# Performance work log

Measured on AMD Instinct MI355X. Metric: run time of the kernel, lower is better.

## Reference

```python
import jax, jax.numpy as jnp
import numpy as np

NMS_PRE_MAXSIZE = 4096
NMS_POST_MAXSIZE = 512
NMS_THRESH = 0.7


def setup_inputs() -> dict:
    key = jax.random.key(0)
    k1, k2, k3, k4, k5 = jax.random.split(key, 5)
    B, N, C = 4, 32768, 3
    # realistic 3D boxes: (x, y, z, dx, dy, dz, heading)
    xy = jax.random.uniform(k1, (B, N, 2), dtype=jnp.float32) * 70.0
    z = jax.random.uniform(k2, (B, N, 1), dtype=jnp.float32) * 4.0 - 2.0
    sizes = jax.random.uniform(k3, (B, N, 3), dtype=jnp.float32) * 3.0 + 1.0
    heading = jax.random.uniform(k4, (B, N, 1), dtype=jnp.float32) * 6.2832 - 3.1416
    batch_box_preds = jnp.concatenate([xy, z, sizes, heading], axis=-1)  # (B,N,7)
    batch_cls_preds = jax.random.uniform(k5, (B, N, C), dtype=jnp.float32)  # (B,N,3)
    return {"batch_box_preds": batch_box_preds, "batch_cls_preds": batch_cls_preds}


def _nms_single(boxes, scores, labels):
    # boxes (N,7), scores (N,), labels (N,) int32
    top_s, idx = jax.lax.top_k(scores, NMS_PRE_MAXSIZE)   # sort desc, keep pre-maxsize
    b = boxes[idx]                                        # (PRE,7)
    l = labels[idx]
    # BEV axis-aligned IoU (reference surrogate for the rotated-BEV CUDA IoU kernel)
    x, y, dx, dy = b[:, 0], b[:, 1], b[:, 3], b[:, 4]
    x1, x2 = x - 0.5 * dx, x + 0.5 * dx
    y1, y2 = y - 0.5 * dy, y + 0.5 * dy
    area = dx * dy
    ix = jnp.maximum(0.0, jnp.minimum(x2[:, None], x2[None, :]) - jnp.maximum(x1[:, None], x1[None, :]))
    iy = jnp.maximum(0.0, jnp.minimum(y2[:, None], y2[None, :]) - jnp.maximum(y1[:, None], y1[None, :]))
    inter = ix * iy
    iou = jax.lax.stop_gradient(inter / (area[:, None] + area[None, :] - inter + 1e-6))

    ar = jnp.arange(NMS_PRE_MAXSIZE)

    def body(i, keep):
        sup = (iou[i] > NMS_THRESH) & (ar > i) & keep[i]
        return keep & ~sup

    keep = jax.lax.fori_loop(0, NMS_PRE_MAXSIZE, body, jnp.ones(NMS_PRE_MAXSIZE, bool))

    # pack first NMS_POST_MAXSIZE kept boxes into fixed-size zero-padded outputs
    rank = jnp.cumsum(keep) - 1
    valid = keep & (rank < NMS_POST_MAXSIZE)
    pos = jnp.where(valid, rank, NMS_POST_MAXSIZE)  # invalid -> scratch row
    rois = jnp.zeros((NMS_POST_MAXSIZE + 1, 7), b.dtype).at[pos].set(b)[:NMS_POST_MAXSIZE]
    sc = jnp.zeros((NMS_POST_MAXSIZE + 1,), top_s.dtype).at[pos].set(top_s)[:NMS_POST_MAXSIZE]
    lb = jnp.zeros((NMS_POST_MAXSIZE + 1,), jnp.int32).at[pos].set(l)[:NMS_POST_MAXSIZE]
    return rois, sc, lb


def reference(batch_box_preds, batch_cls_preds):
    # per-box max score / argmax class (torch.max(cls_preds, dim=1) per sample)
    roi_scores_all = jnp.max(batch_cls_preds, axis=-1)                 # (B,N)
    roi_labels_all = jnp.argmax(batch_cls_preds, axis=-1).astype(jnp.int32)
    rois, roi_scores, roi_labels = jax.vmap(_nms_single)(batch_box_preds, roi_scores_all, roi_labels_all)
    return rois, roi_scores, roi_labels + 1  # labels shifted by +1 as in proposal_layer
```

## Files before the change

kernel.cpp:

```cpp
#include <hip/hip_runtime.h>
#include <stdint.h>

#define BB 4
#define NN 32768
#define PRE 4096
#define POST 512
#define NMS_TH 0.7f
#define MIDCAP 8192
#define P1G 16

typedef unsigned long long u64;
typedef unsigned int u32;

__device__ __forceinline__ u32 orderable(float f) {
  u32 u = __float_as_uint(f);
  return (u & 0x80000000u) ? ~u : (u | 0x80000000u);
}
__device__ __forceinline__ float unorderable(u32 o) {
  u32 u = (o & 0x80000000u) ? (o & 0x7fffffffu) : ~o;
  return __uint_as_float(u);
}
__device__ __forceinline__ u32 bucket_of(float s) {
  u32 v = (u32)(s * 2147483648.0f);
  u32 bk = v >> 20;
  return bk > 2047u ? 2047u : bk;
}
__device__ __forceinline__ u64 readlane64(u64 v, int l) {
  u32 lo = (u32)__builtin_amdgcn_readlane((int)(u32)v, l);
  u32 hi = (u32)__builtin_amdgcn_readlane((int)(u32)(v >> 32), l);
  return ((u64)hi << 32) | lo;
}

__global__ void zero_kernel(u32* __restrict__ hist, u32* __restrict__ cnt_mid) {
  int t = blockIdx.x * 256 + threadIdx.x;
  if (t < BB * 2048) hist[t] = 0;
  if (t < BB) cnt_mid[t] = 0;
}

__global__ __launch_bounds__(256) void score_hist_kernel(const float* __restrict__ cls,
                                                         int* __restrict__ labels,
                                                         u64* __restrict__ keys,
                                                         u32* __restrict__ hist) {
  __shared__ u32 lh[2048];
  for (int t = threadIdx.x; t < 2048; t += 256) lh[t] = 0;
  __syncthreads();
  int g = blockIdx.x * 256 + threadIdx.x;
  const float* c = cls + (size_t)g * 3;
  float s = c[0]; int l = 0;
  float c1 = c[1], c2 = c[2];
  if (c1 > s) { s = c1; l = 1; }
  if (c2 > s) { s = c2; l = 2; }
  int n = g & (NN - 1);
  keys[g] = ((u64)orderable(s) << 32) | (u32)(~(u32)n);
  labels[g] = l;
  atomicAdd(&lh[bucket_of(s)], 1u);
  __syncthreads();
  int b = blockIdx.x >> 7;
  for (int t = threadIdx.x; t < 2048; t += 256) {
    u32 v = lh[t];
    if (v) atomicAdd(&hist[b * 2048 + t], v);
  }
}

__global__ __launch_bounds__(256) void select_kernel(const u32* __restrict__ hist,
                                                     u32* __restrict__ selinfo,
                                                     u32* __restrict__ sfxBuf,
                                                     u32* __restrict__ cursor) {
  __shared__ u32 sfx[2048];
  int b = blockIdx.x;
  for (int t = threadIdx.x; t < 2048; t += 256) sfx[t] = hist[b * 2048 + t];
  __syncthreads();
  for (int d = 1; d < 2048; d <<= 1) {
    u32 v[8];
#pragma unroll
    for (int i = 0; i < 8; ++i) {
      int t = threadIdx.x + i * 256;
      v[i] = (t + d < 2048) ? sfx[t + d] : 0;
    }
    __syncthreads();
#pragma unroll
    for (int i = 0; i < 8; ++i) sfx[threadIdx.x + i * 256] += v[i];
    __syncthreads();
  }
  for (int t = threadIdx.x; t < 2048; t += 256) {
    u32 above = (t + 1 < 2048) ? sfx[t + 1] : 0;
    sfxBuf[b * 2048 + t] = sfx[t];
    cursor[b * 2048 + t] = above;
    if (above < PRE && sfx[t] >= PRE) { selinfo[b * 2] = (u32)t; selinfo[b * 2 + 1] = above; }
  }
}

__global__ __launch_bounds__(256) void compact_kernel(const u64* __restrict__ keys,
                                                      const u32* __restrict__ selinfo,
                                                      u32* __restrict__ cursor,
                                                      u64* __restrict__ sel, u64* __restrict__ mid,
                                                      u32* __restrict__ cnt_mid) {
  int g = blockIdx.x * 256 + threadIdx.x;
  int b = g >> 15;
  u64 key = keys[g];
  u32 bk = bucket_of(unorderable((u32)(key >> 32)));
  u32 T = selinfo[b * 2];
  if (bk > T) {
    u32 p = atomicAdd(&cursor[b * 2048 + bk], 1u);
    sel[((size_t)b << 12) + p] = key;
  } else if (bk == T) {
    u32 p = atomicAdd(&cnt_mid[b], 1u);
    if (p < MIDCAP) mid[(size_t)b * MIDCAP + p] = key;
  }
}

__global__ __launch_bounds__(64) void bsort_kernel(u64* __restrict__ sel, u64* __restrict__ mid,
                                                   const u32* __restrict__ sfxBuf,
                                                   const u32* __restrict__ selinfo,
                                                   const u32* __restrict__ cnt_mid,
                                                   const float* __restrict__ boxes,
                                                   const int* __restrict__ labels,
                                                   float* __restrict__ topBox,
                                                   float4* __restrict__ P,
                                                   float* __restrict__ AR,
                                                   float* __restrict__ topS,
                                                   int* __restrict__ topL) {
  int t = blockIdx.x & 2047;
  int b = blockIdx.x >> 11;
  int lane = threadIdx.x;
  u32 T = selinfo[b * 2];
  if ((u32)t < T) return;
  u64* selB = sel + ((size_t)b << 12);
  u32 start, end;
  if ((u32)t == T) {
    u32 C1 = selinfo[b * 2 + 1];
    int need = PRE - (int)C1;
    int M = (int)cnt_mid[b]; if (M > MIDCAP) M = MIDCAP;
    u64* midB = mid + (size_t)b * MIDCAP;
    for (int r = 0; r < need; ++r) {
      u64 best = 0; int bi = -1;
      for (int q = lane; q < M; q += 64) {
        u64 v = midB[q];
        if (v > best) { best = v; bi = q; }
      }
#pragma unroll
      for (int d = 32; d > 0; d >>= 1) {
        u64 ob = __shfl_xor(best, d, 64);
        int oi = __shfl_xor(bi, d, 64);
        if (ob > best) { best = ob; bi = oi; }
      }
      if (lane == 0) selB[C1 + r] = best;
      if (bi >= 0 && lane == (bi & 63)) midB[bi] = 0;
    }
    start = C1; end = PRE;
  } else {
    start = (t < 2047) ? sfxBuf[b * 2048 + t + 1] : 0u;
    end = sfxBuf[b * 2048 + t];
    int n = (int)(end - start);
    if (n > 64) {
      for (int r = 0; r < n - 1; ++r) {
        u64 best = 0; int bi = -1;
        for (int q = r + lane; q < n; q += 64) {
          u64 v = selB[start + q];
          if (v > best) { best = v; bi = q; }
        }
#pragma unroll
        for (int d = 32; d > 0; d >>= 1) {
          u64 ob = __shfl_xor(best, d, 64);
          int oi = __shfl_xor(bi, d, 64);
          if (ob > best) { best = ob; bi = oi; }
        }
        if (lane == 0) {
          u64 tmp = selB[start + r];
          selB[start + r] = best;
          selB[start + bi] = tmp;
        }
      }
    } else if (n > 1) {
      u64 v = (lane < n) ? selB[start + lane] : 0ULL;
#pragma unroll
      for (int k = 2; k <= 64; k <<= 1) {
#pragma unroll
        for (int j = k >> 1; j > 0; j >>= 1) {
          u64 o = __shfl_xor(v, j, 64);
          bool up = ((lane & k) == 0);
          bool first = ((lane & j) == 0);
          u64 mx = v > o ? v : o, mn = v > o ? o : v;
          v = (first == up) ? mx : mn;
        }
      }
      if (lane < n) selB[start + lane] = v;
    }
  }
  __builtin_amdgcn_s_waitcnt(0);
  for (u32 pos = start + lane; pos < end; pos += 64) {
    u64 key = selB[pos];
    u32 n = ~(u32)key;
    size_t src = (size_t)b * NN + n;
    const float* bx = boxes + src * 7;
    float x = bx[0], y = bx[1], dx = bx[3], dy = bx[4];
    size_t gidx = ((size_t)b << 12) + pos;
    float* tb = topBox + gidx * 7;
#pragma unroll
    for (int c = 0; c < 7; ++c) tb[c] = bx[c];
    float4 p;
    p.x = x - 0.5f * dx; p.z = x + 0.5f * dx;
    p.y = y - 0.5f * dy; p.w = y + 0.5f * dy;
    P[gidx] = p;
    AR[gidx] = dx * dy;
    topS[gidx] = unorderable((u32)(key >> 32));
    topL[gidx] = labels[src];
  }
}

__device__ __forceinline__ void mask_tile(int b, int rb, int w, int lane,
                                          const float4* __restrict__ P,
                                          const float* __restrict__ AR,
                                          u64* __restrict__ maskT,
                                          u64* __restrict__ diag) {
  int base = b << 12;
  int row = (rb << 6) + lane;
  float4 rp = P[base + row];
  float rar = AR[base + row];
  const float4* __restrict__ Pcol = P + base + (w << 6);
  const float* __restrict__ ARcol = AR + base + (w << 6);
  u64 bits = 0;
  float margMin = 1.0f;
#pragma unroll 8
  for (int k = 0; k < 64; ++k) {
    float4 cb = Pcol[k];
    float ca = ARcol[k];
    float ix = fminf(rp.z, cb.z) - fmaxf(rp.x, cb.x); ix = fmaxf(0.0f, ix);
    float iy = fminf(rp.w, cb.w) - fmaxf(rp.y, cb.y); iy = fmaxf(0.0f, iy);
    float inter = ix * iy;
    float denom = ((rar + ca) - inter) + 1e-6f;
    float t = 0.7f * denom;
    bits |= ((u64)(inter > t ? 1u : 0u)) << k;
    margMin = fminf(margMin, fabsf(inter - t) - 2e-5f * t);
  }
  if (__any(margMin <= 0.0f)) {
    bits = 0;
    for (int k = 0; k < 64; ++k) {
      float4 cb = Pcol[k];
      float ca = ARcol[k];
      float ix = fminf(rp.z, cb.z) - fmaxf(rp.x, cb.x); ix = fmaxf(0.0f, ix);
      float iy = fminf(rp.w, cb.w) - fmaxf(rp.y, cb.y); iy = fmaxf(0.0f, iy);
      float inter = ix * iy;
      float denom = ((rar + ca) - inter) + 1e-6f;
      bits |= ((u64)(((inter / denom) > NMS_TH) ? 1u : 0u)) << k;
    }
  }
  maskT[((size_t)(b * 64 + w)) * PRE + row] = bits;
  if (w == rb) diag[base + row] = bits;
}

__global__ __launch_bounds__(256) void mask1_kernel(const float4* __restrict__ P,
                                                    const float* __restrict__ AR,
                                                    u64* __restrict__ maskT,
                                                    u64* __restrict__ diag) {
  int b = blockIdx.y;
  int ti = blockIdx.x * 4 + (threadIdx.x >> 6);
  int lane = threadIdx.x & 63;
  int rb = 0;
  while (rb < P1G - 1 && (64 * (rb + 1) - ((rb + 1) * rb) / 2) <= ti) ++rb;
  int w = rb + (ti - (64 * rb - (rb * (rb - 1)) / 2));
  mask_tile(b, rb, w, lane, P, AR, maskT, diag);
}

__global__ __launch_bounds__(256) void mask2_kernel(const float4* __restrict__ P,
                                                    const float* __restrict__ AR,
                                                    u64* __restrict__ maskT,
                                                    u64* __restrict__ diag,
                                                    const u32* __restrict__ doneFlag) {
  int b = blockIdx.y;
  if (doneFlag[b]) return;
  int ti = blockIdx.x * 4 + (threadIdx.x >> 6);
  int lane = threadIdx.x & 63;
  int rr = 0;
  while (rr < 47 && (48 * (rr + 1) - ((rr + 1) * rr) / 2) <= ti) ++rr;
  int rb = rr + P1G;
  int w = rb + (ti - (48 * rr - (rr * (rr - 1)) / 2));
  mask_tile(b, rb, w, lane, P, AR, maskT, diag);
}

__global__ __launch_bounds__(64, 1) void scan_kernel(const u64* __restrict__ maskT,
                                                     const u64* __restrict__ diag,
                                                     const float* __restrict__ topBox,
                                                     const float* __restrict__ topS,
                                                     const int* __restrict__ topL,
                                                     float* __restrict__ out,
                                                     u64* __restrict__ rState,
                                                     u64* __restrict__ kwState,
                                                     u32* __restrict__ nkState,
                                                     u32* __restrict__ doneFlag,
                                                     int phase) {
  __shared__ u64 kwLDS[64];
  int b = blockIdx.x;
  int lane = threadIdx.x;
  if (phase == 1 && doneFlag[b]) return;
  const u64* m = maskT + (size_t)b * 64 * PRE;
  const u64* dg = diag + (size_t)b * PRE;
  u64 r; int nk, gs, ge;
  if (phase == 0) {
    kwLDS[lane] = 0; r = 0; nk = 0; gs = 0; ge = P1G;
  } else {
    kwLDS[lane] = (lane < P1G) ? kwState[b * 64 + lane] : 0;
    r = rState[b * 64 + lane]; nk = nkState[b]; gs = P1G; ge = 64;
  }
  __syncthreads();
  bool done = false;
  u64 d_next = dg[(size_t)gs * 64 + lane];
  for (int g = gs; g < ge; ++g) {
    u64 d_cur = d_next;
    if (g + 1 < ge) d_next = dg[(size_t)(g + 1) * 64 + lane];
    u64 sup = readlane64(r, g);
    u64 keep;
    u64 anyd = __ballot(d_cur != 0ULL);
    if (anyd == 0ULL) {
      keep = ~sup;
    } else {
      keep = 0;
#pragma unroll
      for (int k = 0; k < 64; ++k) {
        u64 dk = readlane64(d_cur, k);
        u64 bit = (sup >> k) & 1ULL;
        keep |= (bit ^ 1ULL) << k;
        sup |= (dk & ~((2ULL << k) - 1ULL)) & (bit - 1ULL);
      }
    }
    const ulonglong2* mp = (const ulonglong2*)(m + (size_t)lane * PRE + ((size_t)g << 6));
    u64 acc = 0;
#pragma unroll
    for (int q = 0; q < 32; ++q) {
      ulonglong2 v = mp[q];
      u64 g0 = 0ULL - ((keep >> (2 * q)) & 1ULL);
      u64 g1 = 0ULL - ((keep >> (2 * q + 1)) & 1ULL);
      acc |= (v.x & g0) | (v.y & g1);
    }
    r |= acc;
    if (lane == 0) kwLDS[g] = keep;
    nk += (int)__popcll(keep);
    if (nk >= POST) { done = true; break; }
  }
  __syncthreads();
  if (phase == 0 && !done) {
    rState[b * 64 + lane] = r;
    if (lane < P1G) kwState[b * 64 + lane] = kwLDS[lane];
    if (lane == 0) { nkState[b] = nk; doneFlag[b] = 0; }
    return;
  }
  if (phase == 0 && lane == 0) doneFlag[b] = 1;
  u64 kw = kwLDS[lane];
  int cnt = __popcll(kw);
  int pfx = cnt;
#pragma unroll
  for (int d = 1; d < 64; d <<= 1) {
    int up = __shfl_up(pfx, d, 64);
    if (lane >= d) pfx += up;
  }
  int total = __shfl(pfx, 63, 64);
  int pos = pfx - cnt;
  float* outR = out;
  float* outS = out + BB * POST * 7;
  float* outL = outS + BB * POST;
  while (kw) {
    int t = __ffsll((long long)kw) - 1;
    kw &= kw - 1;
    if (pos < POST) {
      int i = (lane << 6) + t;
      int g = (b << 9) + pos;
      const float* tb = topBox + ((size_t)(b << 12) + i) * 7;
#pragma unroll
      for (int c = 0; c < 7; ++c) outR[(size_t)g * 7 + c] = tb[c];
      outS[g] = topS[(b << 12) + i];
      outL[g] = (float)(topL[(b << 12) + i] + 1);
    }
    ++pos;
  }
  int fin = total < POST ? total : POST;
  for (int s = fin + lane; s < POST; s += 64) {
    int g = (b << 9) + s;
#pragma unroll
    for (int c = 0; c < 7; ++c) outR[(size_t)g * 7 + c] = 0.0f;
    outS[g] = 0.0f;
    outL[g] = 1.0f;
  }
}

extern "C" void kernel_launch(void* const* d_in, const int* in_sizes, int n_in,
                              void* d_out, int out_size, void* d_ws, size_t ws_size,
                              hipStream_t stream) {
  const float* boxes = (const float*)d_in[0];
  const float* cls   = (const float*)d_in[1];
  float* out = (float*)d_out;

  char* p = (char*)d_ws;
  auto take = [&](size_t bytes) { char* r = p; p += (bytes + 255) & ~(size_t)255; return (void*)r; };
  u64*   keys    = (u64*)  take((size_t)BB * NN * 8);
  int*   labels  = (int*)  take((size_t)BB * NN * 4);
  u32*   hist    = (u32*)  take((size_t)BB * 2048 * 4);
  u32*   selinfo = (u32*)  take((size_t)BB * 2 * 4);
  u32*   sfxBuf  = (u32*)  take((size_t)BB * 2048 * 4);
  u32*   cursor  = (u32*)  take((size_t)BB * 2048 * 4);
  u32*   cnt_mid = (u32*)  take((size_t)BB * 4);
  u64*   sel     = (u64*)  take((size_t)BB * PRE * 8);
  u64*   mid     = (u64*)  take((size_t)BB * MIDCAP * 8);
  float* topBox  = (float*)take((size_t)BB * PRE * 7 * 4);
  float4* Pb     = (float4*)take((size_t)BB * PRE * 16);
  float* AR      = (float*)take((size_t)BB * PRE * 4);
  float* topS    = (float*)take((size_t)BB * PRE * 4);
  int*   topL    = (int*)  take((size_t)BB * PRE * 4);
  u64*   maskT   = (u64*)  take((size_t)BB * 64 * PRE * 8);
  u64*   diagBuf = (u64*)  take((size_t)BB * PRE * 8);
  u64*   rState  = (u64*)  take((size_t)BB * 64 * 8);
  u64*   kwState = (u64*)  take((size_t)BB * 64 * 8);
  u32*   nkState = (u32*)  take((size_t)BB * 4);
  u32*   doneFlg = (u32*)  take((size_t)BB * 4);

  zero_kernel<<<32, 256, 0, stream>>>(hist, cnt_mid);
  score_hist_kernel<<<BB * NN / 256, 256, 0, stream>>>(cls, labels, keys, hist);
  select_kernel<<<BB, 256, 0, stream>>>(hist, selinfo, sfxBuf, cursor);
  compact_kernel<<<BB * NN / 256, 256, 0, stream>>>(keys, selinfo, cursor, sel, mid, cnt_mid);
  bsort_kernel<<<BB * 2048, 64, 0, stream>>>(sel, mid, sfxBuf, selinfo, cnt_mid,
                                             boxes, labels, topBox, Pb, AR, topS, topL);
  mask1_kernel<<<dim3(226, BB), 256, 0, stream>>>(Pb, AR, maskT, diagBuf);
  scan_kernel<<<BB, 64, 0, stream>>>(maskT, diagBuf, topBox, topS, topL, out,
                                     rState, kwState, nkState, doneFlg, 0);
  mask2_kernel<<<dim3(294, BB), 256, 0, stream>>>(Pb, AR, maskT, diagBuf, doneFlg);
  scan_kernel<<<BB, 64, 0, stream>>>(maskT, diagBuf, topBox, topS, topL, out,
                                     rState, kwState, nkState, doneFlg, 1);
}
```

Baseline: 106.4 us.

## Skip mask loads in NMS scan for rows with no off-diagonal overlaps

During mask construction, each off-diagonal tile now ballots which rows have any overlap bits and atomically ORs that into a per-row-block bitmap. The serial scan kernel reads this bitmap and, for each group, only loads the mask words of kept rows that actually have off-diagonal overlaps, iterating set bits instead of streaming all 32 ulonglong2 loads. This targets the memory latency in the single-wave sequential scan, which is the critical path. It adds atomics in the mask kernels and a data-dependent loop with scattered 8-byte loads in the scan.

```diff
diff --git a/kernel.cpp b/kernel.cpp
--- a/kernel.cpp
+++ b/kernel.cpp
@@ -31,9 +31,11 @@
   return ((u64)hi << 32) | lo;
 }
 
-__global__ void zero_kernel(u32* __restrict__ hist, u32* __restrict__ cnt_mid) {
+__global__ void zero_kernel(u32* __restrict__ hist, u32* __restrict__ cnt_mid,
+                            u64* __restrict__ rowAnyBm) {
   int t = blockIdx.x * 256 + threadIdx.x;
   if (t < BB * 2048) hist[t] = 0;
+  if (t < BB * 64) rowAnyBm[t] = 0;
   if (t < BB) cnt_mid[t] = 0;
 }
 
@@ -212,7 +214,8 @@
                                           const float4* __restrict__ P,
                                           const float* __restrict__ AR,
                                           u64* __restrict__ maskT,
-                                          u64* __restrict__ diag) {
+                                          u64* __restrict__ diag,
+                                          u64* __restrict__ rowAnyBm) {
   int base = b << 12;
   int row = (rb << 6) + lane;
   float4 rp = P[base + row];
@@ -247,25 +250,32 @@
   }
   maskT[((size_t)(b * 64 + w)) * PRE + row] = bits;
   if (w == rb) diag[base + row] = bits;
+  else {
+    u64 anyw = __ballot(bits != 0ULL);
+    if (lane == 0 && anyw)
+      atomicOr((unsigned long long*)&rowAnyBm[b * 64 + rb], anyw);
+  }
 }
 
 __global__ __launch_bounds__(256) void mask1_kernel(const float4* __restrict__ P,
                                                     const float* __restrict__ AR,
                                                     u64* __restrict__ maskT,
-                                                    u64* __restrict__ diag) {
+                                                    u64* __restrict__ diag,
+                                                    u64* __restrict__ rowAnyBm) {
   int b = blockIdx.y;
   int ti = blockIdx.x * 4 + (threadIdx.x >> 6);
   int lane = threadIdx.x & 63;
   int rb = 0;
   while (rb < P1G - 1 && (64 * (rb + 1) - ((rb + 1) * rb) / 2) <= ti) ++rb;
   int w = rb + (ti - (64 * rb - (rb * (rb - 1)) / 2));
-  mask_tile(b, rb, w, lane, P, AR, maskT, diag);
+  mask_tile(b, rb, w, lane, P, AR, maskT, diag, rowAnyBm);
 }
 
 __global__ __launch_bounds__(256) void mask2_kernel(const float4* __restrict__ P,
                                                     const float* __restrict__ AR,
                                                     u64* __restrict__ maskT,
                                                     u64* __restrict__ diag,
+                                                    u64* __restrict__ rowAnyBm,
                                                     const u32* __restrict__ doneFlag) {
   int b = blockIdx.y;
   if (doneFlag[b]) return;
@@ -275,11 +285,12 @@
   while (rr < 47 && (48 * (rr + 1) - ((rr + 1) * rr) / 2) <= ti) ++rr;
   int rb = rr + P1G;
   int w = rb + (ti - (48 * rr - (rr * (rr - 1)) / 2));
-  mask_tile(b, rb, w, lane, P, AR, maskT, diag);
+  mask_tile(b, rb, w, lane, P, AR, maskT, diag, rowAnyBm);
 }
 
 __global__ __launch_bounds__(64, 1) void scan_kernel(const u64* __restrict__ maskT,
                                                      const u64* __restrict__ diag,
+                                                     const u64* __restrict__ rowAnyBm,
                                                      const float* __restrict__ topBox,
                                                      const float* __restrict__ topS,
                                                      const int* __restrict__ topL,
@@ -295,6 +306,7 @@
   if (phase == 1 && doneFlag[b]) return;
   const u64* m = maskT + (size_t)b * 64 * PRE;
   const u64* dg = diag + (size_t)b * PRE;
+  u64 rowAnyW = rowAnyBm[b * 64 + lane];
   u64 r; int nk, gs, ge;
   if (phase == 0) {
     kwLDS[lane] = 0; r = 0; nk = 0; gs = 0; ge = P1G;
@@ -323,16 +335,16 @@
         sup |= (dk & ~((2ULL << k) - 1ULL)) & (bit - 1ULL);
       }
     }
-    const ulonglong2* mp = (const ulonglong2*)(m + (size_t)lane * PRE + ((size_t)g << 6));
-    u64 acc = 0;
-#pragma unroll
-    for (int q = 0; q < 32; ++q) {
-      ulonglong2 v = mp[q];
-      u64 g0 = 0ULL - ((keep >> (2 * q)) & 1ULL);
-      u64 g1 = 0ULL - ((keep >> (2 * q + 1)) & 1ULL);
-      acc |= (v.x & g0) | (v.y & g1);
-    }
-    r |= acc;
+    u64 need = keep & readlane64(rowAnyW, g);
+    if (need) {
+      u64 accr = 0;
+      do {
+        int t = __ffsll((long long)need) - 1;
+        need &= need - 1;
+        accr |= m[(size_t)lane * PRE + (size_t)(g << 6) + t];
+      } while (need);
+      r |= accr;
+    }
     if (lane == 0) kwLDS[g] = keep;
     nk += (int)__popcll(keep);
     if (nk >= POST) { done = true; break; }
@@ -407,21 +419,22 @@
   int*   topL    = (int*)  take((size_t)BB * PRE * 4);
   u64*   maskT   = (u64*)  take((size_t)BB * 64 * PRE * 8);
   u64*   diagBuf = (u64*)  take((size_t)BB * PRE * 8);
+  u64*   rowAny  = (u64*)  take((size_t)BB * 64 * 8);
   u64*   rState  = (u64*)  take((size_t)BB * 64 * 8);
   u64*   kwState = (u64*)  take((size_t)BB * 64 * 8);
   u32*   nkState = (u32*)  take((size_t)BB * 4);
   u32*   doneFlg = (u32*)  take((size_t)BB * 4);
 
-  zero_kernel<<<32, 256, 0, stream>>>(hist, cnt_mid);
+  zero_kernel<<<32, 256, 0, stream>>>(hist, cnt_mid, rowAny);
   score_hist_kernel<<<BB * NN / 256, 256, 0, stream>>>(cls, labels, keys, hist);
   select_kernel<<<BB, 256, 0, stream>>>(hist, selinfo, sfxBuf, cursor);
   compact_kernel<<<BB * NN / 256, 256, 0, stream>>>(keys, selinfo, cursor, sel, mid, cnt_mid);
   bsort_kernel<<<BB * 2048, 64, 0, stream>>>(sel, mid, sfxBuf, selinfo, cnt_mid,
                                              boxes, labels, topBox, Pb, AR, topS, topL);
-  mask1_kernel<<<dim3(226, BB), 256, 0, stream>>>(Pb, AR, maskT, diagBuf);
-  scan_kernel<<<BB, 64, 0, stream>>>(maskT, diagBuf, topBox, topS, topL, out,
+  mask1_kernel<<<dim3(226, BB), 256, 0, stream>>>(Pb, AR, maskT, diagBuf, rowAny);
+  scan_kernel<<<BB, 64, 0, stream>>>(maskT, diagBuf, rowAny, topBox, topS, topL, out,
                                      rState, kwState, nkState, doneFlg, 0);
-  mask2_kernel<<<dim3(294, BB), 256, 0, stream>>>(Pb, AR, maskT, diagBuf, doneFlg);
-  scan_kernel<<<BB, 64, 0, stream>>>(maskT, diagBuf, topBox, topS, topL, out,
+  mask2_kernel<<<dim3(294, BB), 256, 0, stream>>>(Pb, AR, maskT, diagBuf, rowAny, doneFlg);
+  scan_kernel<<<BB, 64, 0, stream>>>(maskT, diagBuf, rowAny, topBox, topS, topL, out,
                                      rState, kwState, nkState, doneFlg, 1);
 }
```

Result: faster. 101.9 us (-4.3%).
